# Kernel tuning notes

Measured on AMD Instinct MI355X. Metric: run time of the kernel, lower is better.

## Reference

```python
import jax, jax.numpy as jnp
import numpy as np

BETA = 0.01
NUM_EMBEDDINGS = 8192
EMBEDDING_DIM = 512


def setup_inputs() -> dict:
    key = jax.random.key(0)
    k1, k2 = jax.random.split(key)
    inputs = jax.random.normal(k1, (16, 2048, EMBEDDING_DIM), dtype=jnp.float32)
    # nn.Embedding weight init: uniform(-1/K, 1/K)
    lim = 1.0 / NUM_EMBEDDINGS
    codebook = jax.random.uniform(k2, (NUM_EMBEDDINGS, EMBEDDING_DIM),
                                  dtype=jnp.float32, minval=-lim, maxval=lim)
    return {"inputs": inputs, "codebook": codebook}


def reference(inputs, codebook):
    D = codebook.shape[1]
    x = inputs.reshape(-1, D)  # [N, D]
    distances = (jnp.sum(x * x, axis=1, keepdims=True)
                 + jnp.sum(codebook * codebook, axis=1)
                 - 2.0 * jnp.einsum('nd,kd->nk', x, codebook))
    encoding_indices = jnp.argmin(distances, axis=1)  # [N]
    quantized = codebook[encoding_indices].reshape(inputs.shape)
    sg = jax.lax.stop_gradient
    mse = lambda a, b: jnp.mean((a - b) ** 2)
    commitment_loss = mse(sg(quantized), inputs) + BETA * mse(quantized, sg(inputs))
    # straight-through estimator
    quantized_st = inputs + sg(quantized - inputs)
    return quantized_st, commitment_loss, encoding_indices
```

## Files before the change

kernel.cpp:

```cpp
#include <hip/hip_runtime.h>
#include <hip/hip_bf16.h>
#include <hip/hip_fp16.h>

typedef unsigned short ushortT;
typedef _Float16 half8 __attribute__((ext_vector_type(8)));
typedef float f32x4 __attribute__((ext_vector_type(4)));

#define N_ROWS   32768
#define DIM      512
#define K_CODES  8192
#define BETA     0.01f

#define LOSS_OFF 16777216
#define IDX_OFF  16777217

#define SC_XH_F      0
#define SC_EH_F      8388608
#define SC_GCODE_F   10485760
#define SC_GCNT_F    11010048
#define SC_FIXMIN_F  11042816
#define SC_FIXLIST_F 11108352

#define WS_XX_OFF     0
#define WS_IDX_OFF    32768
#define WS_PART_OFF   65536
#define WS_CNT_OFF    73728

#define FLT_BIG 3.402823466e+38f
#define W_ACC   0.08192f
#define W_FILT  0.09192f
#define GCAP    16

typedef __attribute__((address_space(1))) const unsigned int GUI;
typedef __attribute__((address_space(3))) unsigned int LUI;
__device__ __forceinline__ void gload16(const void* g, void* l) {
    __builtin_amdgcn_global_load_lds((GUI*)g, (LUI*)l, 16, 0, 0);
}

__global__ __launch_bounds__(256) void vq_prep(const float* __restrict__ x,
                                               const float* __restrict__ cb,
                                               ushortT* __restrict__ xh,
                                               ushortT* __restrict__ eh,
                                               float* __restrict__ xx) {
    __shared__ float l[4][512];
    const size_t gid = (size_t)blockIdx.x * 256 + threadIdx.x;
    const size_t off8 = gid * 8;
    const bool isX = (blockIdx.x < 8192);
    const float* src;
    ushortT* dst;
    float sc;
    if (isX) { src = x + off8; dst = xh + off8; sc = 1.0f; }
    else { size_t o = off8 - 16777216UL; src = cb + o; dst = eh + o; sc = 1024.0f; }
    float4 v0 = *reinterpret_cast<const float4*>(src);
    float4 v1 = *reinterpret_cast<const float4*>(src + 4);
    union { ushortT s[8]; uint4 v; } u;
    u.s[0] = __half_as_ushort(__float2half(v0.x * sc));
    u.s[1] = __half_as_ushort(__float2half(v0.y * sc));
    u.s[2] = __half_as_ushort(__float2half(v0.z * sc));
    u.s[3] = __half_as_ushort(__float2half(v0.w * sc));
    u.s[4] = __half_as_ushort(__float2half(v1.x * sc));
    u.s[5] = __half_as_ushort(__float2half(v1.y * sc));
    u.s[6] = __half_as_ushort(__float2half(v1.z * sc));
    u.s[7] = __half_as_ushort(__float2half(v1.w * sc));
    *reinterpret_cast<uint4*>(dst) = u.v;
    if (isX) {
        const int wave = threadIdx.x >> 6;
        const int lane = threadIdx.x & 63;
        float4 q0 = make_float4(v0.x * v0.x, v0.y * v0.y, v0.z * v0.z, v0.w * v0.w);
        float4 q1 = make_float4(v1.x * v1.x, v1.y * v1.y, v1.z * v1.z, v1.w * v1.w);
        *reinterpret_cast<float4*>(&l[wave][lane * 8]) = q0;
        *reinterpret_cast<float4*>(&l[wave][lane * 8 + 4]) = q1;
        __syncthreads();
        if (lane == 0) {
            float B[4];
#pragma unroll
            for (int q = 0; q < 4; ++q) {
                const float* a = &l[wave][q * 128];
                float r0 = a[0], r1 = a[1], r2 = a[2], r3 = a[3];
                float r4 = a[4], r5 = a[5], r6 = a[6], r7 = a[7];
                for (int i = 8; i < 128; i += 8) {
                    r0 += a[i + 0]; r1 += a[i + 1]; r2 += a[i + 2]; r3 += a[i + 3];
                    r4 += a[i + 4]; r5 += a[i + 5]; r6 += a[i + 6]; r7 += a[i + 7];
                }
                B[q] = ((r0 + r1) + (r2 + r3)) + ((r4 + r5) + (r6 + r7));
            }
            xx[blockIdx.x * 4 + wave] = (B[0] + B[1]) + (B[2] + B[3]);
        }
    }
}

#define BM 128
#define BN 256
#define BKH 64
#define KHALF 4096
#define NSTEP 128

__global__ __launch_bounds__(512, 4) void vq_margmin(
    const ushortT* __restrict__ xh, const ushortT* __restrict__ eh,
    unsigned* __restrict__ gCode, unsigned* __restrict__ gCnt,
    int* __restrict__ fixcnt, int* __restrict__ fixlist) {
    __shared__ ushortT Rs[BM * BKH];
    __shared__ ushortT Cs[BN * BKH];
    float* v1L        = (float*)&Rs[0];
    float* rowThr     = (float*)&Rs[1024];
    unsigned* candCnt = (unsigned*)&Rs[1280];
    int* flagL        = (int*)&Rs[1536];
    unsigned* candList = (unsigned*)&Rs[1792];

    const int t = threadIdx.x;
    const int l = t & 63;
    const int wid = t >> 6;
    const int wr = wid >> 2;
    const int wc = wid & 3;
    const int lr = l & 15;
    const int lg = l >> 4;
    const int rowBase = (blockIdx.x >> 1) * BM;
    const int kbase = (blockIdx.x & 1) * KHALF;

    const ushortT* rSrc0; const ushortT* rSrc1;
    const ushortT* cSrc0; const ushortT* cSrc1; const ushortT* cSrc2; const ushortT* cSrc3;
    int rD0, rD1, cD0, cD1, cD2, cD3;
    {
        int f0 = t,        r0 = f0 >> 3, gs0 = (f0 & 7) ^ (r0 & 7);
        int f1 = t + 512,  r1 = f1 >> 3, gs1 = (f1 & 7) ^ (r1 & 7);
        int f2 = t + 1024, r2 = f2 >> 3, gs2 = (f2 & 7) ^ (r2 & 7);
        int f3 = t + 1536, r3 = f3 >> 3, gs3 = (f3 & 7) ^ (r3 & 7);
        rSrc0 = xh + (size_t)(rowBase + r0) * DIM + gs0 * 8;
        rSrc1 = xh + (size_t)(rowBase + r1) * DIM + gs1 * 8;
        rD0 = f0 * 8; rD1 = f1 * 8;
        cSrc0 = eh + (size_t)(kbase + r0) * DIM + gs0 * 8;
        cSrc1 = eh + (size_t)(kbase + r1) * DIM + gs1 * 8;
        cSrc2 = eh + (size_t)(kbase + r2) * DIM + gs2 * 8;
        cSrc3 = eh + (size_t)(kbase + r3) * DIM + gs3 * 8;
        cD0 = f0 * 8; cD1 = f1 * 8; cD2 = f2 * 8; cD3 = f3 * 8;
    }
    int cB0 = (wc * 64 + 0 * 16 + lr) * 64, cB1 = (wc * 64 + 1 * 16 + lr) * 64;
    int cB2 = (wc * 64 + 2 * 16 + lr) * 64, cB3 = (wc * 64 + 3 * 16 + lr) * 64;
    int rB0 = (wr * 64 + 0 * 16 + lr) * 64, rB1 = (wr * 64 + 1 * 16 + lr) * 64;
    int rB2 = (wr * 64 + 2 * 16 + lr) * 64, rB3 = (wr * 64 + 3 * 16 + lr) * 64;

    float v1[4], v2m[4], v3m[4];
    int i1[4], i2[4];
#pragma unroll
    for (int nf = 0; nf < 4; ++nf) {
        v1[nf] = -FLT_BIG; v2m[nf] = -FLT_BIG; v3m[nf] = -FLT_BIG;
        i1[nf] = 0; i2[nf] = 0;
    }

    f32x4 acc[4][4];

#define STAGE(stp) do {                                                        \
    int kt_ = ((stp) & 7) * BKH;                                               \
    size_t cAdd_ = (size_t)((stp) >> 3) * BN * DIM + kt_;                      \
    gload16(rSrc0 + kt_, &Rs[rD0]);                                            \
    gload16(rSrc1 + kt_, &Rs[rD1]);                                            \
    gload16(cSrc0 + cAdd_, &Cs[cD0]);                                          \
    gload16(cSrc1 + cAdd_, &Cs[cD1]);                                          \
    gload16(cSrc2 + cAdd_, &Cs[cD2]);                                          \
    gload16(cSrc3 + cAdd_, &Cs[cD3]);                                          \
} while (0)

    for (int step = 0; step < NSTEP; ++step) {
        if ((step & 7) == 0) {
#pragma unroll
            for (int mf = 0; mf < 4; ++mf)
#pragma unroll
                for (int nf = 0; nf < 4; ++nf)
                    acc[mf][nf] = (f32x4){0.f, 0.f, 0.f, 0.f};
        }
        __syncthreads();
        STAGE(step);
        __syncthreads();
#pragma unroll
        for (int kk = 0; kk < 2; ++kk) {
            const int sl = ((kk << 2) + lg) ^ (lr & 7);
            half8 a0 = *reinterpret_cast<const half8*>(&Cs[cB0 + sl * 8]);
            half8 a1 = *reinterpret_cast<const half8*>(&Cs[cB1 + sl * 8]);
            half8 a2 = *reinterpret_cast<const half8*>(&Cs[cB2 + sl * 8]);
            half8 a3 = *reinterpret_cast<const half8*>(&Cs[cB3 + sl * 8]);
            half8 b0 = *reinterpret_cast<const half8*>(&Rs[rB0 + sl * 8]);
            half8 b1 = *reinterpret_cast<const half8*>(&Rs[rB1 + sl * 8]);
            half8 b2 = *reinterpret_cast<const half8*>(&Rs[rB2 + sl * 8]);
            half8 b3 = *reinterpret_cast<const half8*>(&Rs[rB3 + sl * 8]);
            acc[0][0] = __builtin_amdgcn_mfma_f32_16x16x32_f16(a0, b0, acc[0][0], 0, 0, 0);
            acc[0][1] = __builtin_amdgcn_mfma_f32_16x16x32_f16(a0, b1, acc[0][1], 0, 0, 0);
            acc[0][2] = __builtin_amdgcn_mfma_f32_16x16x32_f16(a0, b2, acc[0][2], 0, 0, 0);
            acc[0][3] = __builtin_amdgcn_mfma_f32_16x16x32_f16(a0, b3, acc[0][3], 0, 0, 0);
            acc[1][0] = __builtin_amdgcn_mfma_f32_16x16x32_f16(a1, b0, acc[1][0], 0, 0, 0);
            acc[1][1] = __builtin_amdgcn_mfma_f32_16x16x32_f16(a1, b1, acc[1][1], 0, 0, 0);
            acc[1][2] = __builtin_amdgcn_mfma_f32_16x16x32_f16(a1, b2, acc[1][2], 0, 0, 0);
            acc[1][3] = __builtin_amdgcn_mfma_f32_16x16x32_f16(a1, b3, acc[1][3], 0, 0, 0);
            acc[2][0] = __builtin_amdgcn_mfma_f32_16x16x32_f16(a2, b0, acc[2][0], 0, 0, 0);
            acc[2][1] = __builtin_amdgcn_mfma_f32_16x16x32_f16(a2, b1, acc[2][1], 0, 0, 0);
            acc[2][2] = __builtin_amdgcn_mfma_f32_16x16x32_f16(a2, b2, acc[2][2], 0, 0, 0);
            acc[2][3] = __builtin_amdgcn_mfma_f32_16x16x32_f16(a2, b3, acc[2][3], 0, 0, 0);
            acc[3][0] = __builtin_amdgcn_mfma_f32_16x16x32_f16(a3, b0, acc[3][0], 0, 0, 0);
            acc[3][1] = __builtin_amdgcn_mfma_f32_16x16x32_f16(a3, b1, acc[3][1], 0, 0, 0);
            acc[3][2] = __builtin_amdgcn_mfma_f32_16x16x32_f16(a3, b2, acc[3][2], 0, 0, 0);
            acc[3][3] = __builtin_amdgcn_mfma_f32_16x16x32_f16(a3, b3, acc[3][3], 0, 0, 0);
        }
        if ((step & 7) == 7) {
            const int k0t = step >> 3;
#pragma unroll
            for (int nf = 0; nf < 4; ++nf) {
#pragma unroll
                for (int mf = 0; mf < 4; ++mf) {
                    const int tagB = (k0t << 4) | (mf << 2);
#pragma unroll
                    for (int rr = 0; rr < 4; ++rr) {
                        float s = acc[mf][nf][rr];
                        bool g1 = s > v1[nf];
                        bool g2 = s > v2m[nf];
                        bool g3 = s > v3m[nf];
                        v3m[nf] = g2 ? v2m[nf] : (g3 ? s : v3m[nf]);
                        i2[nf]  = g1 ? i1[nf]  : (g2 ? (tagB | rr) : i2[nf]);
                        v2m[nf] = g1 ? v1[nf]  : (g2 ? s : v2m[nf]);
                        i1[nf]  = g1 ? (tagB | rr) : i1[nf];
                        v1[nf]  = g1 ? s : v1[nf];
                    }
                }
            }
        }
    }
#undef STAGE

    __syncthreads();
#pragma unroll
    for (int nf = 0; nf < 4; ++nf) {
        float v = v1[nf];
        v = fmaxf(v, __shfl_xor(v, 16));
        v = fmaxf(v, __shfl_xor(v, 32));
        if (l < 16) v1L[(wr * 64 + nf * 16 + l) * 4 + wc] = v;
    }
    __syncthreads();
    if (t < BM) {
        float m = fmaxf(fmaxf(v1L[t * 4], v1L[t * 4 + 1]),
                        fmaxf(v1L[t * 4 + 2], v1L[t * 4 + 3]));
        rowThr[t] = m - W_ACC;
        candCnt[t] = 0u;
        flagL[t] = 0;
    }
    __syncthreads();
#pragma unroll
    for (int nf = 0; nf < 4; ++nf) {
        const int row = wr * 64 + nf * 16 + lr;
        const float thr = rowThr[row];
        if (v1[nf] >= thr) {
            unsigned pos = atomicAdd(&candCnt[row], 1u);
            int tg = i1[nf];
            int code = kbase + ((tg >> 4) << 8) + wc * 64 + (((tg >> 2) & 3) << 4) + lg * 4 + (tg & 3);
            unsigned pk = ((unsigned)__half_as_ushort(__float2half(v1[nf])) << 16) | (unsigned)code;
            if (pos < GCAP) candList[row * GCAP + pos] = pk;
            else flagL[row] = 1;
        }
        if (v2m[nf] >= thr) {
            unsigned pos = atomicAdd(&candCnt[row], 1u);
            int tg = i2[nf];
            int code = kbase + ((tg >> 4) << 8) + wc * 64 + (((tg >> 2) & 3) << 4) + lg * 4 + (tg & 3);
            unsigned pk = ((unsigned)__half_as_ushort(__float2half(v2m[nf])) << 16) | (unsigned)code;
            if (pos < GCAP) candList[row * GCAP + pos] = pk;
            else flagL[row] = 1;
        }
        if (v3m[nf] >= thr) flagL[row] = 1;
    }
    __syncthreads();
    if (t < BM) {
        const int grow = rowBase + t;
        unsigned cc = candCnt[t];
        bool ovf = (flagL[t] != 0) || (cc > GCAP);
        if (!ovf) {
            for (unsigned j = 0; j < cc; ++j) {
                unsigned pos = atomicAdd(&gCnt[grow], 1u);
                if (pos < GCAP) gCode[(size_t)grow * GCAP + pos] = candList[t * GCAP + j];
                else ovf = true;
            }
        }
        if (ovf) {
            int p = atomicAdd(fixcnt, 1);
            fixlist[p] = grow;
        }
    }
}

__global__ __launch_bounds__(256) void vq_refine(
    const float* __restrict__ x, const float* __restrict__ cb,
    const float* __restrict__ xx, const unsigned* __restrict__ gCode,
    const unsigned* __restrict__ gCnt, float* __restrict__ outIdxF,
    int* __restrict__ idxI) {
    const int wave = threadIdx.x >> 6;
    const int lane = threadIdx.x & 63;
    const int row = blockIdx.x * 4 + wave;
    const unsigned cc = gCnt[row];
    if (cc == 0u || cc > GCAP) return;
    float gmax = -FLT_BIG;
    for (unsigned c = 0; c < cc; ++c) {
        unsigned e = gCode[(size_t)row * GCAP + c];
        gmax = fmaxf(gmax, __half2float(__ushort_as_half((ushortT)(e >> 16))));
    }
    const float fthr = gmax - W_FILT;
    const float* xr = x + (size_t)row * DIM;
    float4 xa = *reinterpret_cast<const float4*>(xr + lane * 8);
    float4 xb = *reinterpret_cast<const float4*>(xr + lane * 8 + 4);
    const float xxrow = xx[row];
    float best = FLT_BIG;
    int bi = 0x7fffffff;
    for (unsigned c = 0; c < cc; ++c) {
        unsigned e = gCode[(size_t)row * GCAP + c];
        if (__half2float(__ushort_as_half((ushortT)(e >> 16))) < fthr) continue;
        int code = (int)(e & 0xFFFFu);
        const float* er = cb + (size_t)code * DIM;
        float4 ea = *reinterpret_cast<const float4*>(er + lane * 8);
        float4 eb = *reinterpret_cast<const float4*>(er + lane * 8 + 4);
        double p = (double)xa.x * ea.x + (double)xa.y * ea.y
                 + (double)xa.z * ea.z + (double)xa.w * ea.w
                 + (double)xb.x * eb.x + (double)xb.y * eb.y
                 + (double)xb.z * eb.z + (double)xb.w * eb.w;
#pragma unroll
        for (int off = 1; off < 64; off <<= 1) p += __shfl_xor(p, off);
        float sc = xxrow - (float)(2.0 * p);
        if (sc < best || (sc == best && code < bi)) { best = sc; bi = code; }
    }
    if (lane == 0) { idxI[row] = bi; outIdxF[row] = (float)bi; }
}

__global__ __launch_bounds__(256) void vq_fixup_scan(
    const float* __restrict__ x, const float* __restrict__ cb,
    const float* __restrict__ xx, const int* __restrict__ cnt,
    const int* __restrict__ list, unsigned long long* __restrict__ fixmin) {
    const int nflag = *cnt;
    if (nflag == 0) return;
    const int gw = (blockIdx.x * 256 + threadIdx.x) >> 6;
    const int lane = threadIdx.x & 63;
    const int nwaves = gridDim.x * 4;
    const int totalUnits = nflag * 128;
    for (int u = gw; u < totalUnits; u += nwaves) {
        const int row = list[u >> 7];
        const int kb = (u & 127) * 64;
        const float* xr = x + (size_t)row * DIM;
        float4 xa = *reinterpret_cast<const float4*>(xr + lane * 8);
        float4 xb = *reinterpret_cast<const float4*>(xr + lane * 8 + 4);
        const float xxrow = xx[row];
        unsigned long long best = ~0ULL;
        for (int k = kb; k < kb + 64; ++k) {
            const float* er = cb + (size_t)k * DIM;
            float4 ea = *reinterpret_cast<const float4*>(er + lane * 8);
            float4 eb = *reinterpret_cast<const float4*>(er + lane * 8 + 4);
            double p = (double)xa.x * ea.x + (double)xa.y * ea.y
                     + (double)xa.z * ea.z + (double)xa.w * ea.w
                     + (double)xb.x * eb.x + (double)xb.y * eb.y
                     + (double)xb.z * eb.z + (double)xb.w * eb.w;
#pragma unroll
            for (int off = 1; off < 64; off <<= 1) p += __shfl_xor(p, off);
            float sc = xxrow - (float)(2.0 * p);
            unsigned long long key =
                ((unsigned long long)__float_as_uint(sc) << 32) | (unsigned)k;
            best = (key < best) ? key : best;
        }
        if (lane == 0) atomicMin(&fixmin[row], best);
    }
}

__global__ __launch_bounds__(256) void vq_fixup_write(
    const int* __restrict__ cnt, const int* __restrict__ list,
    const unsigned long long* __restrict__ fixmin,
    float* __restrict__ outIdxF, int* __restrict__ idxI) {
    const int i = blockIdx.x * 256 + threadIdx.x;
    if (i >= *cnt) return;
    const int row = list[i];
    const int code = (int)(unsigned)(fixmin[row] & 0xFFFFFFFFULL);
    idxI[row] = code;
    outIdxF[row] = (float)code;
}

__global__ __launch_bounds__(256) void vq_gather_kernel(
    const float* __restrict__ x, const float* __restrict__ cb,
    const int* __restrict__ idxI, float* __restrict__ outQ,
    float* __restrict__ partial) {
    const int wave = threadIdx.x >> 6;
    const int lane = threadIdx.x & 63;
    const int row = blockIdx.x * 4 + wave;
    const int code = idxI[row];
    const float* xr = x + (size_t)row * DIM;
    const float* er = cb + (size_t)code * DIM;
    float* qr = outQ + (size_t)row * DIM;
    float s = 0.f;
#pragma unroll
    for (int i = 0; i < 2; ++i) {
        int d = lane * 8 + i * 4;
        float4 xv = *reinterpret_cast<const float4*>(xr + d);
        float4 ev = *reinterpret_cast<const float4*>(er + d);
        float4 dv = make_float4(ev.x - xv.x, ev.y - xv.y, ev.z - xv.z, ev.w - xv.w);
        *reinterpret_cast<float4*>(qr + d) = ev;
        s += dv.x * dv.x + dv.y * dv.y + dv.z * dv.z + dv.w * dv.w;
    }
#pragma unroll
    for (int off = 32; off > 0; off >>= 1) s += __shfl_xor(s, off);
    __shared__ float ws4[4];
    if (lane == 0) ws4[wave] = s;
    __syncthreads();
    if (threadIdx.x == 0)
        partial[blockIdx.x] = (ws4[0] + ws4[1]) + (ws4[2] + ws4[3]);
}

__global__ __launch_bounds__(256) void vq_loss_kernel(const float* __restrict__ partial,
                                                      float* __restrict__ outLoss) {
    float s = 0.f;
    for (int i = threadIdx.x; i < 8192; i += 256) s += partial[i];
    __shared__ float sm[256];
    sm[threadIdx.x] = s;
    __syncthreads();
    for (int off = 128; off > 0; off >>= 1) {
        if (threadIdx.x < off) sm[threadIdx.x] += sm[threadIdx.x + off];
        __syncthreads();
    }
    if (threadIdx.x == 0)
        outLoss[0] = sm[0] * (1.0f + BETA) / 16777216.0f;
}

extern "C" void kernel_launch(void* const* d_in, const int* in_sizes, int n_in,
                              void* d_out, int out_size, void* d_ws, size_t ws_size,
                              hipStream_t stream) {
    const float* x = (const float*)d_in[0];
    const float* cb = (const float*)d_in[1];
    float* out = (float*)d_out;

    ushortT* xh = (ushortT*)out;
    ushortT* eh = (ushortT*)(out + SC_EH_F);
    unsigned* gCode = (unsigned*)(out + SC_GCODE_F);
    unsigned* gCnt = (unsigned*)(out + SC_GCNT_F);
    unsigned long long* fixmin = (unsigned long long*)(out + SC_FIXMIN_F);
    int* fixlist = (int*)(out + SC_FIXLIST_F);

    float* xx = (float*)d_ws + WS_XX_OFF;
    int* idxI = (int*)d_ws + WS_IDX_OFF;
    float* partial = (float*)d_ws + WS_PART_OFF;
    int* fixcnt = (int*)d_ws + WS_CNT_OFF;

    hipMemsetAsync(fixcnt, 0, sizeof(int), stream);
    hipMemsetAsync(gCnt, 0, N_ROWS * sizeof(unsigned), stream);
    hipMemsetAsync(fixmin, 0xFF, N_ROWS * sizeof(unsigned long long), stream);
    hipLaunchKernelGGL(vq_prep, dim3(10240), dim3(256), 0, stream, x, cb, xh, eh, xx);
    hipLaunchKernelGGL(vq_margmin, dim3((N_ROWS / BM) * 2), dim3(512), 0, stream,
                       xh, eh, gCode, gCnt, fixcnt, fixlist);
    hipLaunchKernelGGL(vq_refine, dim3(N_ROWS / 4), dim3(256), 0, stream,
                       x, cb, xx, gCode, gCnt, out + IDX_OFF, idxI);
    hipLaunchKernelGGL(vq_fixup_scan, dim3(2048), dim3(256), 0, stream,
                       x, cb, xx, fixcnt, fixlist, fixmin);
    hipLaunchKernelGGL(vq_fixup_write, dim3(256), dim3(256), 0, stream,
                       fixcnt, fixlist, fixmin, out + IDX_OFF, idxI);
    hipLaunchKernelGGL(vq_gather_kernel, dim3(N_ROWS / 4), dim3(256), 0, stream,
                       x, cb, idxI, out, partial);
    hipLaunchKernelGGL(vq_loss_kernel, dim3(1), dim3(256), 0, stream,
                       partial, out + LOSS_OFF);
}
```

Before: 467.7 us.

## Double-buffer codebook tiles in margmin and fuse memsets into an init kernel

The codebook LDS tile becomes double-buffered, so the next step's codebook loads are issued before the current step's MFMA work, with explicit vmcnt waits and barriers. The row tile stays single-buffered and is reloaded after a barrier at the end of each step. The three hipMemsetAsync calls are replaced by one small init kernel to cut launch and memset overhead. The extra 32KB of LDS may lower occupancy under launch_bounds(512,4), and the hand-counted vmcnt and the barrier ordering are fragile.

```diff
diff --git a/kernel.cpp b/kernel.cpp
--- a/kernel.cpp
+++ b/kernel.cpp
@@ -35,6 +35,15 @@
 typedef __attribute__((address_space(3))) unsigned int LUI;
 __device__ __forceinline__ void gload16(const void* g, void* l) {
     __builtin_amdgcn_global_load_lds((GUI*)g, (LUI*)l, 16, 0, 0);
+}
+
+__global__ __launch_bounds__(256) void vq_init(unsigned* __restrict__ gCnt,
+                                               unsigned long long* __restrict__ fixmin,
+                                               int* __restrict__ fixcnt) {
+    const int i = blockIdx.x * 256 + threadIdx.x;
+    gCnt[i] = 0u;
+    fixmin[i] = ~0ULL;
+    if (i == 0) *fixcnt = 0;
 }
 
 __global__ __launch_bounds__(256) void vq_prep(const float* __restrict__ x,
@@ -100,7 +109,7 @@
     unsigned* __restrict__ gCode, unsigned* __restrict__ gCnt,
     int* __restrict__ fixcnt, int* __restrict__ fixlist) {
     __shared__ ushortT Rs[BM * BKH];
-    __shared__ ushortT Cs[BN * BKH];
+    __shared__ ushortT Cs[2][BN * BKH];
     float* v1L        = (float*)&Rs[0];
     float* rowThr     = (float*)&Rs[1024];
     unsigned* candCnt = (unsigned*)&Rs[1280];
@@ -149,17 +158,24 @@
 
     f32x4 acc[4][4];
 
-#define STAGE(stp) do {                                                        \
+#define STAGE_C(stp, b) do {                                                   \
     int kt_ = ((stp) & 7) * BKH;                                               \
     size_t cAdd_ = (size_t)((stp) >> 3) * BN * DIM + kt_;                      \
+    gload16(cSrc0 + cAdd_, &Cs[b][cD0]);                                       \
+    gload16(cSrc1 + cAdd_, &Cs[b][cD1]);                                       \
+    gload16(cSrc2 + cAdd_, &Cs[b][cD2]);                                       \
+    gload16(cSrc3 + cAdd_, &Cs[b][cD3]);                                       \
+} while (0)
+#define STAGE_R(stp) do {                                                      \
+    int kt_ = ((stp) & 7) * BKH;                                               \
     gload16(rSrc0 + kt_, &Rs[rD0]);                                            \
     gload16(rSrc1 + kt_, &Rs[rD1]);                                            \
-    gload16(cSrc0 + cAdd_, &Cs[cD0]);                                          \
-    gload16(cSrc1 + cAdd_, &Cs[cD1]);                                          \
-    gload16(cSrc2 + cAdd_, &Cs[cD2]);                                          \
-    gload16(cSrc3 + cAdd_, &Cs[cD3]);                                          \
 } while (0)
 
+    STAGE_C(0, 0);
+    STAGE_R(0);
+
+    int cur = 0;
     for (int step = 0; step < NSTEP; ++step) {
         if ((step & 7) == 0) {
 #pragma unroll
@@ -168,16 +184,21 @@
                 for (int nf = 0; nf < 4; ++nf)
                     acc[mf][nf] = (f32x4){0.f, 0.f, 0.f, 0.f};
         }
-        __syncthreads();
-        STAGE(step);
-        __syncthreads();
+        if (step + 1 < NSTEP) {
+            STAGE_C(step + 1, cur ^ 1);
+            asm volatile("s_waitcnt vmcnt(4)" ::: "memory");
+        } else {
+            asm volatile("s_waitcnt vmcnt(0)" ::: "memory");
+        }
+        __builtin_amdgcn_sched_barrier(0);
+        __builtin_amdgcn_s_barrier();
 #pragma unroll
         for (int kk = 0; kk < 2; ++kk) {
             const int sl = ((kk << 2) + lg) ^ (lr & 7);
-            half8 a0 = *reinterpret_cast<const half8*>(&Cs[cB0 + sl * 8]);
-            half8 a1 = *reinterpret_cast<const half8*>(&Cs[cB1 + sl * 8]);
-            half8 a2 = *reinterpret_cast<const half8*>(&Cs[cB2 + sl * 8]);
-            half8 a3 = *reinterpret_cast<const half8*>(&Cs[cB3 + sl * 8]);
+            half8 a0 = *reinterpret_cast<const half8*>(&Cs[cur][cB0 + sl * 8]);
+            half8 a1 = *reinterpret_cast<const half8*>(&Cs[cur][cB1 + sl * 8]);
+            half8 a2 = *reinterpret_cast<const half8*>(&Cs[cur][cB2 + sl * 8]);
+            half8 a3 = *reinterpret_cast<const half8*>(&Cs[cur][cB3 + sl * 8]);
             half8 b0 = *reinterpret_cast<const half8*>(&Rs[rB0 + sl * 8]);
             half8 b1 = *reinterpret_cast<const half8*>(&Rs[rB1 + sl * 8]);
             half8 b2 = *reinterpret_cast<const half8*>(&Rs[rB2 + sl * 8]);
@@ -221,8 +242,12 @@
                 }
             }
         }
-    }
-#undef STAGE
+        __builtin_amdgcn_s_barrier();
+        if (step + 1 < NSTEP) STAGE_R(step + 1);
+        cur ^= 1;
+    }
+#undef STAGE_C
+#undef STAGE_R
 
     __syncthreads();
 #pragma unroll
@@ -436,9 +461,7 @@
     float* partial = (float*)d_ws + WS_PART_OFF;
     int* fixcnt = (int*)d_ws + WS_CNT_OFF;
 
-    hipMemsetAsync(fixcnt, 0, sizeof(int), stream);
-    hipMemsetAsync(gCnt, 0, N_ROWS * sizeof(unsigned), stream);
-    hipMemsetAsync(fixmin, 0xFF, N_ROWS * sizeof(unsigned long long), stream);
+    hipLaunchKernelGGL(vq_init, dim3(128), dim3(256), 0, stream, gCnt, fixmin, fixcnt);
     hipLaunchKernelGGL(vq_prep, dim3(10240), dim3(256), 0, stream, x, cb, xh, eh, xx);
     hipLaunchKernelGGL(vq_margmin, dim3((N_ROWS / BM) * 2), dim3(512), 0, stream,
                        xh, eh, gCode, gCnt, fixcnt, fixlist);
```

Result: slower. 555.1 us (+18.7%).
